# Kernel optimization log

Measured on AMD Instinct MI355X. Metric: run time of the kernel, lower is better.

The kernel has to match this reference:

```python
import jax, jax.numpy as jnp
import numpy as np

N_EMBD = 1024
N_HEAD = 16
LN_EPS = 1e-5

def setup_inputs() -> dict:
    key = jax.random.key(0)
    ks = jax.random.split(key, 12)
    B, T, C = 2, 2048, N_EMBD
    s = lambda k, shape, scale=0.02: (jax.random.normal(k, shape, dtype=jnp.float32) * scale)
    return {
        "x": jax.random.normal(ks[0], (B, T, C), dtype=jnp.float32),
        "ln1_g": jnp.ones((C,), jnp.float32),
        "ln1_b": jnp.zeros((C,), jnp.float32),
        "W_attn": s(ks[1], (C, 3 * C)),
        "b_attn": jnp.zeros((3 * C,), jnp.float32),
        "W_o": s(ks[2], (C, C)),
        "b_o": jnp.zeros((C,), jnp.float32),
        "ln2_g": jnp.ones((C,), jnp.float32),
        "ln2_b": jnp.zeros((C,), jnp.float32),
        "W_fc": s(ks[3], (C, 4 * C)),
        "b_fc": jnp.zeros((4 * C,), jnp.float32),
        "W_fc2": s(ks[4], (4 * C, C)),
        "b_fc2": jnp.zeros((C,), jnp.float32),
    }

def _layernorm(x, g, b):
    mu = jnp.mean(x, axis=-1, keepdims=True)
    var = jnp.mean(jnp.square(x - mu), axis=-1, keepdims=True)
    return (x - mu) * jax.lax.rsqrt(var + LN_EPS) * g + b

def reference(x, ln1_g, ln1_b, W_attn, b_attn, W_o, b_o, ln2_g, ln2_b, W_fc, b_fc, W_fc2, b_fc2):
    B, T, C = x.shape
    H, D = N_HEAD, C // N_HEAD
    # ---- attention branch (use_cache=False: T_total == T, causal mask) ----
    h = _layernorm(x, ln1_g, ln1_b)
    qkv = h @ W_attn + b_attn                       # [B,T,3C]
    q, k, v = jnp.split(qkv, 3, axis=-1)
    q = q.reshape(B, T, H, D).transpose(0, 2, 1, 3)  # [B,H,T,D]
    k = k.reshape(B, T, H, D).transpose(0, 2, 1, 3)
    v = v.reshape(B, T, H, D).transpose(0, 2, 1, 3)
    w = jnp.einsum('bhqd,bhkd->bhqk', q, k) / jnp.sqrt(jnp.float32(D))  # [B,H,T,T]
    causal = jnp.tril(jnp.ones((T, T), dtype=bool))
    w = jnp.where(causal, w, jnp.float32(-jnp.inf))
    w = jax.nn.softmax(w, axis=-1)
    y = jnp.einsum('bhqk,bhkd->bhqd', w, v)          # [B,H,T,D]
    y = y.transpose(0, 2, 1, 3).reshape(B, T, C)
    x = x + (y @ W_o + b_o)
    # ---- MLP branch ----
    h2 = _layernorm(x, ln2_g, ln2_b)
    h2 = jax.nn.gelu(h2 @ W_fc + b_fc, approximate=True)  # tanh approx, matches nn.GELU('tanh')
    x = x + (h2 @ W_fc2 + b_fc2)
    return x
```

## Files before the change

kernel.cpp:

```cpp
#include <hip/hip_runtime.h>


typedef unsigned short u16;
typedef unsigned int u32;
typedef __attribute__((ext_vector_type(8))) short v8s;
typedef __attribute__((ext_vector_type(4))) float v4f;

#define GAS __attribute__((address_space(1)))
#define LAS __attribute__((address_space(3)))

__device__ __forceinline__ u16 f2bf(float f) {
  u32 u = __float_as_uint(f);
  u = (u + 0x7FFF + ((u >> 16) & 1)) >> 16;
  return (u16)u;
}
__device__ __forceinline__ float bf2f(u16 h) {
  return __uint_as_float(((u32)h) << 16);
}
__device__ __forceinline__ float fast_tanh(float x) {
  return 1.f - 2.f / (1.f + __expf(2.f * x));
}

__global__ __launch_bounds__(256)
void wtrans(const float* __restrict__ W, u16* __restrict__ Wt, int K, int N) {
  __shared__ float tile[32][33];
  const int n0 = blockIdx.x << 5, k0 = blockIdx.y << 5;
  const int r = threadIdx.x >> 5, c = threadIdx.x & 31;
#pragma unroll
  for (int i = 0; i < 4; ++i)
    tile[r + 8 * i][c] = W[(size_t)(k0 + r + 8 * i) * N + n0 + c];
  __syncthreads();
#pragma unroll
  for (int i = 0; i < 4; ++i)
    Wt[(size_t)(n0 + r + 8 * i) * K + k0 + c] = f2bf(tile[c][r + 8 * i]);
}

__global__ __launch_bounds__(256)
void ln_bf16(const float* __restrict__ x, const float* __restrict__ g,
             const float* __restrict__ be, u16* __restrict__ out) {
  constexpr int C = 1024;
  const int row = blockIdx.x, t = threadIdx.x;
  const float4 v = ((const float4*)(x + (size_t)row * C))[t];
  float s = v.x + v.y + v.z + v.w;
#pragma unroll
  for (int m = 32; m >= 1; m >>= 1) s += __shfl_xor(s, m);
  __shared__ float red[4], red2[4];
  if ((t & 63) == 0) red[t >> 6] = s;
  __syncthreads();
  const float mu = (red[0] + red[1] + red[2] + red[3]) * (1.f / C);
  const float dx = v.x - mu, dy = v.y - mu, dz = v.z - mu, dw = v.w - mu;
  float s2 = dx * dx + dy * dy + dz * dz + dw * dw;
#pragma unroll
  for (int m = 32; m >= 1; m >>= 1) s2 += __shfl_xor(s2, m);
  if ((t & 63) == 0) red2[t >> 6] = s2;
  __syncthreads();
  const float var = (red2[0] + red2[1] + red2[2] + red2[3]) * (1.f / C);
  const float rs = rsqrtf(var + 1e-5f);
  const int c = t << 2;
  u16 o0 = f2bf(dx * rs * g[c + 0] + be[c + 0]);
  u16 o1 = f2bf(dy * rs * g[c + 1] + be[c + 1]);
  u16 o2 = f2bf(dz * rs * g[c + 2] + be[c + 2]);
  u16 o3 = f2bf(dw * rs * g[c + 3] + be[c + 3]);
  uint2 pk;
  pk.x = (u32)o0 | ((u32)o1 << 16);
  pk.y = (u32)o2 | ((u32)o3 << 16);
  *(uint2*)(out + (size_t)row * C + c) = pk;
}

template <int EPI>
__global__ __launch_bounds__(256)
void gemm_bt(const u16* __restrict__ A, const u16* __restrict__ Bt,
             const float* __restrict__ bias, const float* __restrict__ res,
             void* __restrict__ outp, int M, int N, int K) {
  __shared__ u16 As[128 * 32];
  __shared__ u16 Bs[128 * 32];
  const int tid = threadIdx.x;
  const int wave = tid >> 6, lane = tid & 63;
  const int m0 = blockIdx.y << 7, n0 = blockIdx.x << 7;

  v4f acc[4][4];
  const v4f vz = {0.f, 0.f, 0.f, 0.f};
#pragma unroll
  for (int i = 0; i < 4; ++i)
#pragma unroll
    for (int j = 0; j < 4; ++j) acc[i][j] = vz;

  const int wm = (wave >> 1) << 6, wn = (wave & 1) << 6;
  const int sr = lane >> 2;
  const int sc = (lane & 3) << 3;
  const int fr = lane & 15;
  const int fk = (lane >> 4) << 3;
  const int c0 = wave << 1;

  u16* lA0 = As + (c0 + 0) * 512;
  u16* lA1 = As + (c0 + 1) * 512;
  u16* lB0 = Bs + (c0 + 0) * 512;
  u16* lB1 = Bs + (c0 + 1) * 512;
  const u16* gA0 = A + (size_t)(m0 + c0 * 16 + sr) * K + sc;
  const u16* gA1 = A + (size_t)(m0 + c0 * 16 + 16 + sr) * K + sc;
  const u16* gB0 = Bt + (size_t)(n0 + c0 * 16 + sr) * K + sc;
  const u16* gB1 = Bt + (size_t)(n0 + c0 * 16 + 16 + sr) * K + sc;

  for (int k0 = 0; k0 < K; k0 += 32) {
    __builtin_amdgcn_global_load_lds((GAS const u32*)(gA0 + k0), (LAS u32*)lA0, 16, 0, 0);
    __builtin_amdgcn_global_load_lds((GAS const u32*)(gA1 + k0), (LAS u32*)lA1, 16, 0, 0);
    __builtin_amdgcn_global_load_lds((GAS const u32*)(gB0 + k0), (LAS u32*)lB0, 16, 0, 0);
    __builtin_amdgcn_global_load_lds((GAS const u32*)(gB1 + k0), (LAS u32*)lB1, 16, 0, 0);
    __syncthreads();
    v8s af[4], bfr[4];
#pragma unroll
    for (int mi = 0; mi < 4; ++mi)
      af[mi] = *(const v8s*)&As[(wm + mi * 16 + fr) * 32 + fk];
#pragma unroll
    for (int ni = 0; ni < 4; ++ni)
      bfr[ni] = *(const v8s*)&Bs[(wn + ni * 16 + fr) * 32 + fk];
#pragma unroll
    for (int mi = 0; mi < 4; ++mi)
#pragma unroll
      for (int ni = 0; ni < 4; ++ni)
        acc[mi][ni] = __builtin_amdgcn_mfma_f32_16x16x32_bf16(af[mi], bfr[ni], acc[mi][ni], 0, 0, 0);
    __syncthreads();
  }

  const int er = (lane >> 4) << 2;
#pragma unroll
  for (int mi = 0; mi < 4; ++mi) {
#pragma unroll
    for (int ni = 0; ni < 4; ++ni) {
      const int col = n0 + wn + ni * 16 + fr;
      const float bcol = bias[col];
#pragma unroll
      for (int r = 0; r < 4; ++r) {
        const int row = m0 + wm + mi * 16 + er + r;
        float v = acc[mi][ni][r] + bcol;
        if constexpr (EPI == 1) {
          const float t = fast_tanh(0.7978845608028654f * (v + 0.044715f * v * v * v));
          v = 0.5f * v * (1.f + t);
        }
        if constexpr (EPI == 2) {
          v += res[(size_t)row * N + col];
          ((float*)outp)[(size_t)row * N + col] = v;
        } else {
          ((u16*)outp)[(size_t)row * N + col] = f2bf(v);
        }
      }
    }
  }
}

template <int EPI>
__global__ __launch_bounds__(256)
void gemm_bt_n64(const u16* __restrict__ A, const u16* __restrict__ Bt,
                 const float* __restrict__ bias, const float* __restrict__ res,
                 void* __restrict__ outp, int M, int N, int K) {
  __shared__ u16 As[2][128 * 32];
  __shared__ u16 Bs[2][64 * 32];
  const int tid = threadIdx.x;
  const int wave = tid >> 6, lane = tid & 63;
  const int m0 = blockIdx.y << 7, n0 = blockIdx.x << 6;

  v4f acc[4][2];
  const v4f vz = {0.f, 0.f, 0.f, 0.f};
#pragma unroll
  for (int i = 0; i < 4; ++i)
#pragma unroll
    for (int j = 0; j < 2; ++j) acc[i][j] = vz;

  const int wm = (wave >> 1) << 6, wn = (wave & 1) << 5;
  const int sr = lane >> 2;
  const int sc = (lane & 3) << 3;
  const int fr = lane & 15;
  const int fk = (lane >> 4) << 3;

  const u16* gA0 = A + (size_t)(m0 + wave * 32 + sr) * K + sc;
  const u16* gA1 = A + (size_t)(m0 + wave * 32 + 16 + sr) * K + sc;
  const u16* gB0 = Bt + (size_t)(n0 + wave * 16 + sr) * K + sc;
  const int aoff = wave * 1024;
  const int boff = wave * 512;

  const int nk = K >> 5;
  {
    __builtin_amdgcn_global_load_lds((GAS const u32*)gA0, (LAS u32*)(As[0] + aoff), 16, 0, 0);
    __builtin_amdgcn_global_load_lds((GAS const u32*)gA1, (LAS u32*)(As[0] + aoff + 512), 16, 0, 0);
    __builtin_amdgcn_global_load_lds((GAS const u32*)gB0, (LAS u32*)(Bs[0] + boff), 16, 0, 0);
  }
  for (int kt = 0; kt < nk; ++kt) {
    __syncthreads();
    if (kt + 1 < nk) {
      const int k0 = (kt + 1) << 5;
      const int nb = (kt + 1) & 1;
      __builtin_amdgcn_global_load_lds((GAS const u32*)(gA0 + k0), (LAS u32*)(As[nb] + aoff), 16, 0, 0);
      __builtin_amdgcn_global_load_lds((GAS const u32*)(gA1 + k0), (LAS u32*)(As[nb] + aoff + 512), 16, 0, 0);
      __builtin_amdgcn_global_load_lds((GAS const u32*)(gB0 + k0), (LAS u32*)(Bs[nb] + boff), 16, 0, 0);
    }
    const u16* Ab = As[kt & 1];
    const u16* Bb = Bs[kt & 1];
    v8s af[4], bfr[2];
#pragma unroll
    for (int mi = 0; mi < 4; ++mi)
      af[mi] = *(const v8s*)&Ab[(wm + mi * 16 + fr) * 32 + fk];
#pragma unroll
    for (int ni = 0; ni < 2; ++ni)
      bfr[ni] = *(const v8s*)&Bb[(wn + ni * 16 + fr) * 32 + fk];
#pragma unroll
    for (int mi = 0; mi < 4; ++mi)
#pragma unroll
      for (int ni = 0; ni < 2; ++ni)
        acc[mi][ni] = __builtin_amdgcn_mfma_f32_16x16x32_bf16(af[mi], bfr[ni], acc[mi][ni], 0, 0, 0);
  }

  const int er = (lane >> 4) << 2;
#pragma unroll
  for (int mi = 0; mi < 4; ++mi) {
#pragma unroll
    for (int ni = 0; ni < 2; ++ni) {
      const int col = n0 + wn + ni * 16 + fr;
      const float bcol = bias[col];
#pragma unroll
      for (int r = 0; r < 4; ++r) {
        const int row = m0 + wm + mi * 16 + er + r;
        float v = acc[mi][ni][r] + bcol;
        if constexpr (EPI == 1) {
          const float t = fast_tanh(0.7978845608028654f * (v + 0.044715f * v * v * v));
          v = 0.5f * v * (1.f + t);
        }
        if constexpr (EPI == 2) {
          v += res[(size_t)row * N + col];
          ((float*)outp)[(size_t)row * N + col] = v;
        } else {
          ((u16*)outp)[(size_t)row * N + col] = f2bf(v);
        }
      }
    }
  }
}

__global__ __launch_bounds__(256)
void transpose_v(const u16* __restrict__ qkv, u16* __restrict__ Vt) {
  __shared__ u16 tile[64][65];
  const int t0 = blockIdx.x << 6;
  const int bh = blockIdx.y;
  const int b = bh >> 4, h = bh & 15;
  const int r4 = threadIdx.x >> 6, c = threadIdx.x & 63;
#pragma unroll
  for (int i = 0; i < 16; ++i) {
    const int r = r4 * 16 + i;
    tile[r][c] = qkv[(size_t)(b * 2048 + t0 + r) * 3072 + 2048 + h * 64 + c];
  }
  __syncthreads();
#pragma unroll
  for (int i = 0; i < 16; ++i) {
    const int d = r4 * 16 + i;
    Vt[(size_t)bh * 64 * 2048 + (size_t)d * 2048 + t0 + c] = tile[c][d];
  }
}

constexpr int PSTR = 88;

template <bool MASKED>
__device__ __forceinline__ void attn_sub(
    const v8s (&kf)[4][2], const v8s (&vfr)[4][2], const v8s (&qf)[2],
    v4f (&ot)[4], float& m_i, float& l_i, u16* __restrict__ pw,
    const int kb, const int qrow, const int fr, const int fg) {
  const v4f vz = {0.f, 0.f, 0.f, 0.f};
  v4f st[4];
#pragma unroll
  for (int ks = 0; ks < 4; ++ks) {
    st[ks] = vz;
    st[ks] = __builtin_amdgcn_mfma_f32_16x16x32_bf16(kf[ks][0], qf[0], st[ks], 0, 0, 0);
    st[ks] = __builtin_amdgcn_mfma_f32_16x16x32_bf16(kf[ks][1], qf[1], st[ks], 0, 0, 0);
  }
  const int q = qrow + fr;
  float e[4][4];
  float mt = -1e30f;
#pragma unroll
  for (int ks = 0; ks < 4; ++ks)
#pragma unroll
    for (int r = 0; r < 4; ++r) {
      float v = st[ks][r] * 0.125f;
      if (MASKED) v = (kb + ks * 16 + fg * 4 + r <= q) ? v : -1e30f;
      e[ks][r] = v;
      mt = fmaxf(mt, v);
    }
  mt = fmaxf(mt, __shfl_xor(mt, 16));
  mt = fmaxf(mt, __shfl_xor(mt, 32));
  const float m_new = fmaxf(m_i, mt);
  const float alpha = __expf(m_i - m_new);
  m_i = m_new;
  float ls = 0.f;
#pragma unroll
  for (int ks = 0; ks < 4; ++ks)
#pragma unroll
    for (int r = 0; r < 4; ++r) {
      e[ks][r] = __expf(e[ks][r] - m_new);
      ls += e[ks][r];
    }
  ls += __shfl_xor(ls, 16);
  ls += __shfl_xor(ls, 32);
  l_i = l_i * alpha + ls;
#pragma unroll
  for (int ds = 0; ds < 4; ++ds) ot[ds] *= alpha;
#pragma unroll
  for (int ks = 0; ks < 4; ++ks) {
    ushort4 pk4;
    pk4.x = f2bf(e[ks][0]);
    pk4.y = f2bf(e[ks][1]);
    pk4.z = f2bf(e[ks][2]);
    pk4.w = f2bf(e[ks][3]);
    *(ushort4*)&pw[fr * PSTR + ks * 16 + fg * 4] = pk4;
  }
  const v8s pf0 = *(const v8s*)&pw[fr * PSTR + fg * 8];
  const v8s pf1 = *(const v8s*)&pw[fr * PSTR + 32 + fg * 8];
#pragma unroll
  for (int ds = 0; ds < 4; ++ds) {
    ot[ds] = __builtin_amdgcn_mfma_f32_16x16x32_bf16(vfr[ds][0], pf0, ot[ds], 0, 0, 0);
    ot[ds] = __builtin_amdgcn_mfma_f32_16x16x32_bf16(vfr[ds][1], pf1, ot[ds], 0, 0, 0);
  }
}

__global__ __launch_bounds__(256)
void attn_kernel(const u16* __restrict__ qkv, const u16* __restrict__ Vt,
                 u16* __restrict__ y) {
  constexpr int T = 2048, D = 64, C = 1024, QS = 3072;
  __shared__ alignas(16) u16 Ktile[2][64 * 64];
  __shared__ alignas(16) u16 Vtile[2][64 * 64];
  __shared__ alignas(16) u16 Pw[4][16 * PSTR];

  const int tid = threadIdx.x, wave = tid >> 6, lane = tid & 63;
  const int fr = lane & 15, fg = lane >> 4;
  const int bh = blockIdx.y, b = bh >> 4, h = bh & 15;
  const int ta = blockIdx.x, tb = 31 - ta;
  const u16* qkvb = qkv + (size_t)b * T * QS + h * 64;
  const u16* Kg = qkvb + 1024;
  const u16* Vh = Vt + (size_t)bh * D * T;
  u16* pw = &Pw[wave][0];

  const int rowA = ta * 64 + wave * 16;
  const int rowB = tb * 64 + wave * 16;

  v8s qfA[2], qfB[2];
#pragma unroll
  for (int dh = 0; dh < 2; ++dh) {
    qfA[dh] = *(const v8s*)&qkvb[(size_t)(rowA + fr) * QS + dh * 32 + fg * 8];
    qfB[dh] = *(const v8s*)&qkvb[(size_t)(rowB + fr) * QS + dh * 32 + fg * 8];
  }

  const v4f vz = {0.f, 0.f, 0.f, 0.f};
  v4f otA[4], otB[4];
#pragma unroll
  for (int ds = 0; ds < 4; ++ds) { otA[ds] = vz; otB[ds] = vz; }
  float mA = -1e30f, lA = 0.f, mB = -1e30f, lB = 0.f;

  const int srow = lane >> 3;
  const int sg0 = lane & 7;

  const int nt = tb + 1;
  {
#pragma unroll
    for (int cc = 0; cc < 2; ++cc) {
      const int r0 = wave * 16 + cc * 8;
      const int rr = r0 + srow;
      const int gg = sg0 ^ (rr & 7);
      __builtin_amdgcn_global_load_lds(
          (GAS const u32*)(Kg + (size_t)rr * QS + gg * 8),
          (LAS u32*)(Ktile[0] + r0 * 64), 16, 0, 0);
      __builtin_amdgcn_global_load_lds(
          (GAS const u32*)(Vh + (size_t)rr * T + gg * 8),
          (LAS u32*)(Vtile[0] + r0 * 64), 16, 0, 0);
    }
  }
  for (int kt = 0; kt < nt; ++kt) {
    __syncthreads();
    if (kt + 1 < nt) {
      const int kb1 = (kt + 1) << 6;
      const int nb = (kt + 1) & 1;
#pragma unroll
      for (int cc = 0; cc < 2; ++cc) {
        const int r0 = wave * 16 + cc * 8;
        const int rr = r0 + srow;
        const int gg = sg0 ^ (rr & 7);
        __builtin_amdgcn_global_load_lds(
            (GAS const u32*)(Kg + (size_t)(kb1 + rr) * QS + gg * 8),
            (LAS u32*)(Ktile[nb] + r0 * 64), 16, 0, 0);
        __builtin_amdgcn_global_load_lds(
            (GAS const u32*)(Vh + (size_t)rr * T + kb1 + gg * 8),
            (LAS u32*)(Vtile[nb] + r0 * 64), 16, 0, 0);
      }
    }
    const u16* Kt = Ktile[kt & 1];
    const u16* Vi = Vtile[kt & 1];
    const int kb = kt << 6;
    const int swz = fr & 7;
    v8s kf[4][2], vfr[4][2];
#pragma unroll
    for (int ks = 0; ks < 4; ++ks) {
      const int rr = ks * 16 + fr;
      kf[ks][0] = *(const v8s*)&Kt[rr * 64 + ((0 + fg) ^ swz) * 8];
      kf[ks][1] = *(const v8s*)&Kt[rr * 64 + ((4 + fg) ^ swz) * 8];
      vfr[ks][0] = *(const v8s*)&Vi[rr * 64 + ((0 + fg) ^ swz) * 8];
      vfr[ks][1] = *(const v8s*)&Vi[rr * 64 + ((4 + fg) ^ swz) * 8];
    }
    if (kt < ta) {
      attn_sub<false>(kf, vfr, qfA, otA, mA, lA, pw, kb, rowA, fr, fg);
      attn_sub<false>(kf, vfr, qfB, otB, mB, lB, pw, kb, rowB, fr, fg);
    } else if (kt == ta) {
      attn_sub<true>(kf, vfr, qfA, otA, mA, lA, pw, kb, rowA, fr, fg);
      attn_sub<false>(kf, vfr, qfB, otB, mB, lB, pw, kb, rowB, fr, fg);
    } else if (kt < tb) {
      attn_sub<false>(kf, vfr, qfB, otB, mB, lB, pw, kb, rowB, fr, fg);
    } else {
      attn_sub<true>(kf, vfr, qfB, otB, mB, lB, pw, kb, rowB, fr, fg);
    }
  }

  const float invA = 1.f / lA, invB = 1.f / lB;
#pragma unroll
  for (int ds = 0; ds < 4; ++ds) {
    ushort4 a4, b4;
    a4.x = f2bf(otA[ds][0] * invA);
    a4.y = f2bf(otA[ds][1] * invA);
    a4.z = f2bf(otA[ds][2] * invA);
    a4.w = f2bf(otA[ds][3] * invA);
    b4.x = f2bf(otB[ds][0] * invB);
    b4.y = f2bf(otB[ds][1] * invB);
    b4.z = f2bf(otB[ds][2] * invB);
    b4.w = f2bf(otB[ds][3] * invB);
    *(ushort4*)&y[(size_t)(b * T + rowA + fr) * C + h * D + ds * 16 + fg * 4] = a4;
    *(ushort4*)&y[(size_t)(b * T + rowB + fr) * C + h * D + ds * 16 + fg * 4] = b4;
  }
}

extern "C" void kernel_launch(void* const* d_in, const int* in_sizes, int n_in,
                              void* d_out, int out_size, void* d_ws, size_t ws_size,
                              hipStream_t stream) {
  const float* x      = (const float*)d_in[0];
  const float* ln1_g  = (const float*)d_in[1];
  const float* ln1_b  = (const float*)d_in[2];
  const float* W_attn = (const float*)d_in[3];
  const float* b_attn = (const float*)d_in[4];
  const float* W_o    = (const float*)d_in[5];
  const float* b_o    = (const float*)d_in[6];
  const float* ln2_g  = (const float*)d_in[7];
  const float* ln2_b  = (const float*)d_in[8];
  const float* W_fc   = (const float*)d_in[9];
  const float* b_fc   = (const float*)d_in[10];
  const float* W_fc2  = (const float*)d_in[11];
  const float* b_fc2  = (const float*)d_in[12];
  float* out = (float*)d_out;
  char* ws = (char*)d_ws;

  const size_t MB = 1u << 20;
  u16* Wattn_t = (u16*)(ws + 0 * MB);
  u16* Wo_t    = (u16*)(ws + 6 * MB);
  u16* Wfc_t   = (u16*)(ws + 8 * MB);
  u16* Wfc2_t  = (u16*)(ws + 16 * MB);
  float* x1    = (float*)(ws + 24 * MB);
  u16* h1      = (u16*)(ws + 40 * MB);
  u16* qkv     = (u16*)(ws + 48 * MB);
  u16* Vt      = (u16*)(ws + 88 * MB);
  u16* yb      = (u16*)(ws + 40 * MB);
  u16* h2      = (u16*)(ws + 48 * MB);
  u16* ab      = (u16*)(ws + 56 * MB);

  wtrans<<<dim3(3072 / 32, 1024 / 32), 256, 0, stream>>>(W_attn, Wattn_t, 1024, 3072);
  wtrans<<<dim3(1024 / 32, 1024 / 32), 256, 0, stream>>>(W_o, Wo_t, 1024, 1024);
  wtrans<<<dim3(4096 / 32, 1024 / 32), 256, 0, stream>>>(W_fc, Wfc_t, 1024, 4096);
  wtrans<<<dim3(1024 / 32, 4096 / 32), 256, 0, stream>>>(W_fc2, Wfc2_t, 4096, 1024);

  ln_bf16<<<4096, 256, 0, stream>>>(x, ln1_g, ln1_b, h1);
  gemm_bt<0><<<dim3(3072 / 128, 4096 / 128), 256, 0, stream>>>(
      h1, Wattn_t, b_attn, nullptr, qkv, 4096, 3072, 1024);
  transpose_v<<<dim3(2048 / 64, 32), 256, 0, stream>>>(qkv, Vt);
  attn_kernel<<<dim3(16, 32), 256, 0, stream>>>(qkv, Vt, yb);
  gemm_bt_n64<2><<<dim3(1024 / 64, 4096 / 128), 256, 0, stream>>>(
      yb, Wo_t, b_o, x, x1, 4096, 1024, 1024);
  ln_bf16<<<4096, 256, 0, stream>>>(x1, ln2_g, ln2_b, h2);
  gemm_bt<1><<<dim3(4096 / 128, 4096 / 128), 256, 0, stream>>>(
      h2, Wfc_t, b_fc, nullptr, ab, 4096, 4096, 1024);
  gemm_bt_n64<2><<<dim3(1024 / 64, 4096 / 128), 256, 0, stream>>>(
      ab, Wfc2_t, b_fc2, x1, out, 4096, 1024, 4096);
}
```

Before: 390.0 us.

## Deepen N64 GEMM LDS pipeline to four stages with explicit vmcnt waits

Replaces the double-buffered LDS pipeline in the 128x64 GEMM with a four-buffer ring that keeps three k-tiles of global-to-LDS loads in flight. The __syncthreads is replaced by partial s_waitcnt vmcnt counts plus s_barrier, so a wave waits only for the oldest tile. The aim is to hide global memory latency better. The cost is double the LDS footprint, which may lower occupancy, and the tail handling depends on exact vmcnt accounting.

```diff
diff --git a/kernel.cpp b/kernel.cpp
--- a/kernel.cpp
+++ b/kernel.cpp
@@ -153,8 +153,8 @@
 void gemm_bt_n64(const u16* __restrict__ A, const u16* __restrict__ Bt,
                  const float* __restrict__ bias, const float* __restrict__ res,
                  void* __restrict__ outp, int M, int N, int K) {
-  __shared__ u16 As[2][128 * 32];
-  __shared__ u16 Bs[2][64 * 32];
+  __shared__ u16 As[4][128 * 32];
+  __shared__ u16 Bs[4][64 * 32];
   const int tid = threadIdx.x;
   const int wave = tid >> 6, lane = tid & 63;
   const int m0 = blockIdx.y << 7, n0 = blockIdx.x << 6;
@@ -179,22 +179,25 @@
   const int boff = wave * 512;
 
   const int nk = K >> 5;
-  {
-    __builtin_amdgcn_global_load_lds((GAS const u32*)gA0, (LAS u32*)(As[0] + aoff), 16, 0, 0);
-    __builtin_amdgcn_global_load_lds((GAS const u32*)gA1, (LAS u32*)(As[0] + aoff + 512), 16, 0, 0);
-    __builtin_amdgcn_global_load_lds((GAS const u32*)gB0, (LAS u32*)(Bs[0] + boff), 16, 0, 0);
-  }
-  for (int kt = 0; kt < nk; ++kt) {
-    __syncthreads();
-    if (kt + 1 < nk) {
-      const int k0 = (kt + 1) << 5;
-      const int nb = (kt + 1) & 1;
-      __builtin_amdgcn_global_load_lds((GAS const u32*)(gA0 + k0), (LAS u32*)(As[nb] + aoff), 16, 0, 0);
-      __builtin_amdgcn_global_load_lds((GAS const u32*)(gA1 + k0), (LAS u32*)(As[nb] + aoff + 512), 16, 0, 0);
-      __builtin_amdgcn_global_load_lds((GAS const u32*)(gB0 + k0), (LAS u32*)(Bs[nb] + boff), 16, 0, 0);
-    }
-    const u16* Ab = As[kt & 1];
-    const u16* Bb = Bs[kt & 1];
+
+#define N64_ISSUE(t, bf)                                                      \
+  do {                                                                        \
+    const int k0_ = (t) << 5;                                                 \
+    __builtin_amdgcn_global_load_lds((GAS const u32*)(gA0 + k0_),             \
+                                     (LAS u32*)(As[bf] + aoff), 16, 0, 0);    \
+    __builtin_amdgcn_global_load_lds((GAS const u32*)(gA1 + k0_),             \
+                                     (LAS u32*)(As[bf] + aoff + 512), 16, 0, 0); \
+    __builtin_amdgcn_global_load_lds((GAS const u32*)(gB0 + k0_),             \
+                                     (LAS u32*)(Bs[bf] + boff), 16, 0, 0);    \
+  } while (0)
+
+  N64_ISSUE(0, 0);
+  N64_ISSUE(1, 1);
+  N64_ISSUE(2, 2);
+
+  auto compute = [&](int kt) __attribute__((always_inline)) {
+    const u16* Ab = As[kt & 3];
+    const u16* Bb = Bs[kt & 3];
     v8s af[4], bfr[2];
 #pragma unroll
     for (int mi = 0; mi < 4; ++mi)
@@ -207,7 +210,21 @@
 #pragma unroll
       for (int ni = 0; ni < 2; ++ni)
         acc[mi][ni] = __builtin_amdgcn_mfma_f32_16x16x32_bf16(af[mi], bfr[ni], acc[mi][ni], 0, 0, 0);
-  }
+  };
+
+  for (int kt = 0; kt < nk - 2; ++kt) {
+    asm volatile("s_waitcnt vmcnt(6)" ::: "memory");
+    __builtin_amdgcn_s_barrier();
+    if (kt + 3 < nk) N64_ISSUE(kt + 3, (kt + 3) & 3);
+    compute(kt);
+  }
+  asm volatile("s_waitcnt vmcnt(3)" ::: "memory");
+  __builtin_amdgcn_s_barrier();
+  compute(nk - 2);
+  asm volatile("s_waitcnt vmcnt(0)" ::: "memory");
+  __builtin_amdgcn_s_barrier();
+  compute(nk - 1);
+#undef N64_ISSUE
 
   const int er = (lane >> 4) << 2;
 #pragma unroll
```

Result: no change. 385.9 us (-1.1%).
